# Optimization experiments

Hardware: AMD Instinct MI355X
Metric: run time of the kernel (lower is better)

The kernel has to match this reference:

```python
import jax, jax.numpy as jnp
import numpy as np

C_QKV = 1024
C_HIDDEN = 64
NUM_HEADS = 16
INF = 1e9


def setup_inputs() -> dict:
    key = jax.random.key(0)
    ks = jax.random.split(key, 10)
    B, S = 2, 2048
    d = C_QKV
    hd = C_HIDDEN * NUM_HEADS
    sc = 0.02
    return {
        "input_qkv": jax.random.normal(ks[0], (B, S, d), jnp.float32),
        "mask": jnp.ones((B, 1, 1, S), jnp.float32),
        "bias": jax.random.normal(ks[1], (1, NUM_HEADS, S, S), jnp.float32) * sc,
        "wq": jax.random.normal(ks[2], (d, hd), jnp.float32) * sc,
        "wk": jax.random.normal(ks[3], (d, hd), jnp.float32) * sc,
        "wv": jax.random.normal(ks[4], (d, hd), jnp.float32) * sc,
        "wg": jax.random.normal(ks[5], (d, hd), jnp.float32) * sc,
        "bg": jnp.zeros((hd,), jnp.float32),
        "wo": jax.random.normal(ks[6], (hd, d), jnp.float32) * sc,
        "bo": jnp.zeros((d,), jnp.float32),
    }


def reference(input_qkv, mask, bias, wq, wk, wv, wg, bg, wo, bo):
    B, S, _ = input_qkv.shape
    H, C = NUM_HEADS, C_HIDDEN
    # projections -> [B, H, S, C]
    q = (input_qkv @ wq).reshape(B, S, H, C).transpose(0, 2, 1, 3)
    k = (input_qkv @ wk).reshape(B, S, H, C).transpose(0, 2, 1, 3)
    v = (input_qkv @ wv).reshape(B, S, H, C).transpose(0, 2, 1, 3)
    q = q / jnp.asarray(C, q.dtype) ** 0.5
    # scores [B, H, S, S] with additive mask and pair bias
    a = jnp.einsum("bhqc,bhkc->bhqk", q, k)
    a = a + (mask - 1.0) * INF + bias
    a = jax.nn.softmax(a, axis=-1)
    o = jnp.einsum("bhqk,bhkc->bhqc", a, v).transpose(0, 2, 1, 3)  # [B,S,H,C]
    gate = jax.nn.sigmoid(input_qkv @ wg + bg).reshape(B, S, H, C)
    o = (o * gate).reshape(B, S, H * C)
    return o @ wo + bo
```

## Files before the change

kernel.cpp:

```cpp
#include <hip/hip_runtime.h>
#include <hip/hip_bf16.h>
#include <stdint.h>

typedef unsigned short u16;
typedef __attribute__((ext_vector_type(8))) short short8;
typedef __attribute__((ext_vector_type(4))) short short4v;
typedef __attribute__((ext_vector_type(4))) float f32x4;

#define MFMA16 __builtin_amdgcn_mfma_f32_16x16x32_bf16

#define GLOAD_LDS16(gsrc, ldst) \
  __builtin_amdgcn_global_load_lds((const __attribute__((address_space(1))) void*)(gsrc), \
                                   (__attribute__((address_space(3))) void*)(ldst), 16, 0, 0)

__device__ __forceinline__ u16 f2bf(float x) {
  union { float f; uint32_t u; } v; v.f = x;
  uint32_t r = v.u + 0x7FFFu + ((v.u >> 16) & 1u);
  return (u16)(r >> 16);
}
__device__ __forceinline__ u16 f2bf_rn(float x) {
  __hip_bfloat16 h = __float2bfloat16(x);
  return *reinterpret_cast<u16*>(&h);
}
__device__ __forceinline__ float bf2f(u16 b) {
  union { uint32_t u; float f; } v; v.u = ((uint32_t)b) << 16;
  return v.f;
}

__global__ __launch_bounds__(256) void convert_bf16_kernel(
    const float* __restrict__ in, u16* __restrict__ out, int n) {
  int i = (blockIdx.x * 256 + threadIdx.x) * 8;
  if (i >= n) return;
  float4 a = *(const float4*)(in + i);
  float4 b = *(const float4*)(in + i + 4);
  short8 t;
  t[0] = (short)f2bf(a.x); t[1] = (short)f2bf(a.y);
  t[2] = (short)f2bf(a.z); t[3] = (short)f2bf(a.w);
  t[4] = (short)f2bf(b.x); t[5] = (short)f2bf(b.y);
  t[6] = (short)f2bf(b.z); t[7] = (short)f2bf(b.w);
  *(short8*)(out + i) = t;
}

__global__ __launch_bounds__(256) void transpose_w64_4(
    const float* __restrict__ w0, const float* __restrict__ w1,
    const float* __restrict__ w2, const float* __restrict__ w3,
    u16* __restrict__ WT) {
  __shared__ float tile[64][68];
  const int t = threadIdx.x;
  const int z = blockIdx.z;
  const float* W = (z == 0) ? w0 : (z == 1) ? w1 : (z == 2) ? w2 : w3;
  u16* dst_base = WT + (size_t)z * 1024 * 1024;
  const int k0 = blockIdx.x * 64, n0 = blockIdx.y * 64;
  {
    int r = t >> 2, c0 = (t & 3) * 16;
    const float* src = W + (size_t)(k0 + r) * 1024 + n0 + c0;
#pragma unroll
    for (int j = 0; j < 16; j += 4) {
      float4 v = *(const float4*)(src + j);
      tile[r][c0 + j + 0] = v.x; tile[r][c0 + j + 1] = v.y;
      tile[r][c0 + j + 2] = v.z; tile[r][c0 + j + 3] = v.w;
    }
  }
  __syncthreads();
  {
    int n = t >> 2, kq = (t & 3) * 16;
    short8 t0, t1;
#pragma unroll
    for (int j = 0; j < 8; ++j)  t0[j] = (short)f2bf(tile[kq + j][n]);
#pragma unroll
    for (int j = 0; j < 8; ++j)  t1[j] = (short)f2bf(tile[kq + 8 + j][n]);
    u16* dst = dst_base + (size_t)(n0 + n) * 1024 + k0 + kq;
    *(short8*)dst = t0;
    *(short8*)(dst + 8) = t1;
  }
}

__global__ __launch_bounds__(256) void transpose_w64(
    const float* __restrict__ W, u16* __restrict__ WT, int KK, int NN) {
  __shared__ float tile[64][68];
  const int t = threadIdx.x;
  const int k0 = blockIdx.x * 64, n0 = blockIdx.y * 64;
  {
    int r = t >> 2, c0 = (t & 3) * 16;
    const float* src = W + (size_t)(k0 + r) * NN + n0 + c0;
#pragma unroll
    for (int j = 0; j < 16; j += 4) {
      float4 v = *(const float4*)(src + j);
      tile[r][c0 + j + 0] = v.x; tile[r][c0 + j + 1] = v.y;
      tile[r][c0 + j + 2] = v.z; tile[r][c0 + j + 3] = v.w;
    }
  }
  __syncthreads();
  {
    int n = t >> 2, kq = (t & 3) * 16;
    short8 t0, t1;
#pragma unroll
    for (int j = 0; j < 8; ++j)  t0[j] = (short)f2bf(tile[kq + j][n]);
#pragma unroll
    for (int j = 0; j < 8; ++j)  t1[j] = (short)f2bf(tile[kq + 8 + j][n]);
    u16* dst = WT + (size_t)(n0 + n) * KK + k0 + kq;
    *(short8*)dst = t0;
    *(short8*)(dst + 8) = t1;
  }
}

__global__ __launch_bounds__(256) void transpose_v64(
    const u16* __restrict__ vin, u16* __restrict__ vout) {
  __shared__ u16 tile[64][80];
  const int t = threadIdx.x;
  const int s0 = blockIdx.x * 64;
  const int bh = blockIdx.y;
  const int b = bh >> 4, h = bh & 15;
  {
    int r = t >> 2, c0 = (t & 3) * 16;
    const u16* src = vin + (size_t)(b * 2048 + s0 + r) * 1024 + h * 64 + c0;
    *(short8*)&tile[r][c0] = *(const short8*)src;
    *(short8*)&tile[r][c0 + 8] = *(const short8*)(src + 8);
  }
  __syncthreads();
  {
    int c = t >> 2, s4 = (t & 3) * 16;
    short8 t0, t1;
#pragma unroll
    for (int j = 0; j < 8; ++j) t0[j] = (short)tile[s4 + j][c];
#pragma unroll
    for (int j = 0; j < 8; ++j) t1[j] = (short)tile[s4 + 8 + j][c];
    u16* dst = vout + (size_t)(bh * 64 + c) * 2048 + s0 + s4;
    *(short8*)dst = t0;
    *(short8*)(dst + 8) = t1;
  }
}

__global__ __launch_bounds__(256) void gemm_bt128(
    const u16* __restrict__ A, const u16* __restrict__ BTbase,
    void* __restrict__ dstbase, const float* __restrict__ bvec, int mode) {
  const int K = 1024;
  const int tid = threadIdx.x, lane = tid & 63, w = tid >> 6;
  const int wr = w >> 1, wc = w & 1;
  const int l15 = lane & 15, lg = lane >> 4;
  const int z = (mode < 0) ? (int)blockIdx.z : mode;
  const u16* BT = (mode < 0) ? BTbase + (size_t)z * 1024 * 1024 : BTbase;
  const int rbase = blockIdx.x * 128;
  const int nbase = blockIdx.y * 128;
  __shared__ u16 lsA[128 * 64];
  __shared__ u16 lsB[128 * 64];
  f32x4 acc[4][4] = {};
  const int col8 = (lane & 7) * 8;
  for (int kt = 0; kt < K / 64; ++kt) {
#pragma unroll
    for (int i = 0; i < 4; ++i) {
      int row = w * 32 + i * 8 + (lane >> 3);
      const u16* sa = A + (size_t)(rbase + row) * K + kt * 64 + col8;
      GLOAD_LDS16(sa, lsA + (w * 32 + i * 8) * 64 + lane * 8);
      const u16* sb = BT + (size_t)(nbase + row) * K + kt * 64 + col8;
      GLOAD_LDS16(sb, lsB + (w * 32 + i * 8) * 64 + lane * 8);
    }
    __syncthreads();
#pragma unroll
    for (int kk = 0; kk < 2; ++kk) {
      short8 af[4], bfr[4];
#pragma unroll
      for (int m = 0; m < 4; ++m)
        af[m] = *(const short8*)&lsA[(wr * 64 + m * 16 + l15) * 64 + kk * 32 + lg * 8];
#pragma unroll
      for (int n = 0; n < 4; ++n)
        bfr[n] = *(const short8*)&lsB[(wc * 64 + n * 16 + l15) * 64 + kk * 32 + lg * 8];
#pragma unroll
      for (int m = 0; m < 4; ++m)
#pragma unroll
        for (int n = 0; n < 4; ++n)
          acc[m][n] = MFMA16(af[m], bfr[n], acc[m][n], 0, 0, 0);
    }
    __syncthreads();
  }
  const int r0 = rbase + wr * 64;
  const int c0 = nbase + wc * 64;
  if (z == 4) {
    float* out = (float*)dstbase;
#pragma unroll
    for (int m = 0; m < 4; ++m)
#pragma unroll
      for (int n = 0; n < 4; ++n)
#pragma unroll
        for (int i = 0; i < 4; ++i) {
          int r = r0 + m * 16 + lg * 4 + i;
          int c = c0 + n * 16 + l15;
          out[(size_t)r * 1024 + c] = acc[m][n][i] + bvec[c];
        }
  } else {
    u16* dq = (u16*)dstbase + (size_t)z * 4096 * 1024;
#pragma unroll
    for (int m = 0; m < 4; ++m)
#pragma unroll
      for (int n = 0; n < 4; ++n)
#pragma unroll
        for (int i = 0; i < 4; ++i) {
          int r = r0 + m * 16 + lg * 4 + i;
          int c = c0 + n * 16 + l15;
          float v = acc[m][n][i];
          if (z == 0) v *= 0.125f;
          else if (z == 3) v = 1.f / (1.f + __expf(-(v + bvec[c])));
          dq[(size_t)r * 1024 + c] = f2bf(v);
        }
  }
}

__global__ __launch_bounds__(256, 2) void attn_kernel(
    const u16* __restrict__ qws, const u16* __restrict__ kws,
    const u16* __restrict__ vt, const u16* __restrict__ gws,
    const float* __restrict__ bias, const float* __restrict__ mask,
    u16* __restrict__ og) {
  const int tid = threadIdx.x;
  const int lane = tid & 63;
  const int w = tid >> 6;
  const int l15 = lane & 15, lg = lane >> 4;
  const int bx = blockIdx.x;
  const int qt = (bx & 7) | ((bx >> 4) << 3);
  const int b = (bx >> 3) & 1;
  const int h = blockIdx.y;

  __shared__ __align__(16) u16 ring[3][8192];
  __shared__ __align__(16) u16 lsP[4][2304];
  __shared__ __align__(16) u16 lsM[2048];

  const float* bias_base = bias + ((size_t)h * 2048 + qt * 128) * 2048;
  const u16* vt_base = vt + (size_t)((b * 16 + h) * 64) * 2048;
  const u16* k_base = kws + (size_t)(b * 2048) * 1024 + h * 64;

  {
    float4 m0 = *(const float4*)(mask + b * 2048 + tid * 8);
    float4 m1 = *(const float4*)(mask + b * 2048 + tid * 8 + 4);
    short8 mm;
    mm[0] = (short)f2bf((m0.x - 1.f) * 1e9f); mm[1] = (short)f2bf((m0.y - 1.f) * 1e9f);
    mm[2] = (short)f2bf((m0.z - 1.f) * 1e9f); mm[3] = (short)f2bf((m0.w - 1.f) * 1e9f);
    mm[4] = (short)f2bf((m1.x - 1.f) * 1e9f); mm[5] = (short)f2bf((m1.y - 1.f) * 1e9f);
    mm[6] = (short)f2bf((m1.z - 1.f) * 1e9f); mm[7] = (short)f2bf((m1.w - 1.f) * 1e9f);
    *(short8*)&lsM[tid * 8] = mm;
  }

  const size_t qrow0 = (size_t)(b * 2048 + qt * 128 + w * 32 + l15) * 1024 + h * 64;
  const size_t qrow1 = qrow0 + 16 * 1024;
  short8 qf00 = *(const short8*)(qws + qrow0 + lg * 8);
  short8 qf01 = *(const short8*)(qws + qrow0 + 32 + lg * 8);
  short8 qf10 = *(const short8*)(qws + qrow1 + lg * 8);
  short8 qf11 = *(const short8*)(qws + qrow1 + 32 + lg * 8);
  asm volatile("" :: "v"(qf00), "v"(qf01), "v"(qf10), "v"(qf11));
  asm volatile("s_waitcnt vmcnt(0)" ::: "memory");
  __builtin_amdgcn_sched_barrier(0);

  f32x4 O[2][4] = {};
  float lacc0 = 0.f, lacc1 = 0.f;
  f32x4 bA0, bA1, bA2, bA3, bA4, bA5, bA6, bA7;
  f32x4 bB0, bB1, bB2, bB3, bB4, bB5, bB6, bB7;
  f32x4 kX0, kX1, vX0, vX1, kY0, kY1, vY0, vY1;

#define STAGE_ISSUE(K0, K1, V0, V1, KW) {                                           \
    int r_ = tid >> 3, cg_ = tid & 7;                                               \
    const u16* kp_ = k_base + (size_t)((KW) * 64 + r_) * 1024 + cg_ * 8;            \
    const u16* vp_ = vt_base + (size_t)r_ * 2048 + (KW) * 64 + cg_ * 8;             \
    asm volatile("global_load_dwordx4 %0, %1, off" : "=v"(K0) : "v"(kp_));          \
    asm volatile("global_load_dwordx4 %0, %1, off" : "=v"(K1) : "v"(kp_ + 32 * 1024)); \
    asm volatile("global_load_dwordx4 %0, %1, off" : "=v"(V0) : "v"(vp_));          \
    asm volatile("global_load_dwordx4 %0, %1, off" : "=v"(V1) : "v"(vp_ + 32 * 2048)); \
  }

#define STAGE_WRITE(SLOT, K0, K1, V0, V1) {                                         \
    int r_ = tid >> 3, cg_ = tid & 7;                                               \
    int d0_ = (r_ * 8 + (cg_ ^ (r_ & 7))) * 8;                                      \
    int r2_ = r_ + 32;                                                              \
    int d1_ = (r2_ * 8 + (cg_ ^ (r2_ & 7))) * 8;                                    \
    *(f32x4*)&ring[SLOT][d0_] = K0;                                                 \
    *(f32x4*)&ring[SLOT][d1_] = K1;                                                 \
    *(f32x4*)&ring[SLOT][4096 + d0_] = V0;                                          \
    *(f32x4*)&ring[SLOT][4096 + d1_] = V1;                                          \
  }

#define BIAS_ISSUE(R0, R1, R2, R3, R4, R5, R6, R7, KW) {                            \
    const float* bp_ = bias_base + (size_t)(w * 32 + l15) * 2048 + (KW) * 64 + lg * 4; \
    asm volatile("global_load_dwordx4 %0, %1, off" : "=v"(R0) : "v"(bp_));          \
    asm volatile("global_load_dwordx4 %0, %1, off" : "=v"(R1) : "v"(bp_ + 16));     \
    asm volatile("global_load_dwordx4 %0, %1, off" : "=v"(R2) : "v"(bp_ + 32));     \
    asm volatile("global_load_dwordx4 %0, %1, off" : "=v"(R3) : "v"(bp_ + 48));     \
    asm volatile("global_load_dwordx4 %0, %1, off" : "=v"(R4) : "v"(bp_ + 16 * 2048)); \
    asm volatile("global_load_dwordx4 %0, %1, off" : "=v"(R5) : "v"(bp_ + 16 * 2048 + 16)); \
    asm volatile("global_load_dwordx4 %0, %1, off" : "=v"(R6) : "v"(bp_ + 16 * 2048 + 32)); \
    asm volatile("global_load_dwordx4 %0, %1, off" : "=v"(R7) : "v"(bp_ + 16 * 2048 + 48)); \
  }

#define COMPUTE(SLOT, KB, X0, X1, X2, X3, X4, X5, X6, X7) {                         \
    const u16* Kc_ = &ring[SLOT][0];                                                \
    const u16* Vc_ = &ring[SLOT][4096];                                             \
    f32x4 bb0[4] = {X0, X1, X2, X3};                                                \
    f32x4 bb1[4] = {X4, X5, X6, X7};                                                \
    f32x4 s_[2][4];                                                                 \
    _Pragma("unroll") for (int kt = 0; kt < 4; ++kt) {                              \
      int krow_ = kt * 16 + l15;                                                    \
      int sw_ = krow_ & 7;                                                          \
      short8 kfa_ = *(const short8*)&Kc_[(krow_ * 8 + (lg ^ sw_)) * 8];             \
      short8 kfb_ = *(const short8*)&Kc_[(krow_ * 8 + ((4 + lg) ^ sw_)) * 8];       \
      short4v mk_ = *(const short4v*)&lsM[(KB) * 64 + kt * 16 + lg * 4];            \
      f32x4 ci0_, ci1_;                                                             \
      _Pragma("unroll") for (int i = 0; i < 4; ++i) {                               \
        float m_ = bf2f((u16)mk_[i]);                                               \
        ci0_[i] = bb0[kt][i] + m_;                                                  \
        ci1_[i] = bb1[kt][i] + m_;                                                  \
      }                                                                             \
      s_[0][kt] = MFMA16(kfa_, qf00, ci0_, 0, 0, 0);                                \
      s_[0][kt] = MFMA16(kfb_, qf01, s_[0][kt], 0, 0, 0);                           \
      s_[1][kt] = MFMA16(kfa_, qf10, ci1_, 0, 0, 0);                                \
      s_[1][kt] = MFMA16(kfb_, qf11, s_[1][kt], 0, 0, 0);                           \
    }                                                                               \
    _Pragma("unroll") for (int kt = 0; kt < 4; ++kt) {                              \
      short4v p0_, p1_;                                                             \
      _Pragma("unroll") for (int i = 0; i < 4; ++i) {                               \
        float e0_ = __expf(s_[0][kt][i]); lacc0 += e0_; p0_[i] = (short)f2bf_rn(e0_); \
        float e1_ = __expf(s_[1][kt][i]); lacc1 += e1_; p1_[i] = (short)f2bf_rn(e1_); \
      }                                                                             \
      *(short4v*)&lsP[w][(l15) * 72 + kt * 16 + lg * 4] = p0_;                      \
      *(short4v*)&lsP[w][(16 + l15) * 72 + kt * 16 + lg * 4] = p1_;                 \
    }                                                                               \
    short8 pf00_ = *(const short8*)&lsP[w][(l15) * 72 + lg * 8];                    \
    short8 pf01_ = *(const short8*)&lsP[w][(l15) * 72 + 32 + lg * 8];               \
    short8 pf10_ = *(const short8*)&lsP[w][(16 + l15) * 72 + lg * 8];               \
    short8 pf11_ = *(const short8*)&lsP[w][(16 + l15) * 72 + 32 + lg * 8];          \
    _Pragma("unroll") for (int cf = 0; cf < 4; ++cf) {                              \
      int c_ = cf * 16 + l15;                                                       \
      int sw_ = c_ & 7;                                                             \
      short8 vf0_ = *(const short8*)&Vc_[(c_ * 8 + (lg ^ sw_)) * 8];                \
      short8 vf1_ = *(const short8*)&Vc_[(c_ * 8 + ((4 + lg) ^ sw_)) * 8];          \
      O[0][cf] = MFMA16(vf0_, pf00_, O[0][cf], 0, 0, 0);                            \
      O[0][cf] = MFMA16(vf1_, pf01_, O[0][cf], 0, 0, 0);                            \
      O[1][cf] = MFMA16(vf0_, pf10_, O[1][cf], 0, 0, 0);                            \
      O[1][cf] = MFMA16(vf1_, pf11_, O[1][cf], 0, 0, 0);                            \
    } }

#define BODY(KB, N, SK0, SK1, SV0, SV1, TK0, TK1, TV0, TV1,                         \
             X0, X1, X2, X3, X4, X5, X6, X7) {                                      \
    if ((KB) + 2 < 32) STAGE_ISSUE(SK0, SK1, SV0, SV1, (KB) + 2);                   \
    COMPUTE((KB) % 3, KB, X0, X1, X2, X3, X4, X5, X6, X7);                          \
    if ((KB) + 2 < 32) BIAS_ISSUE(X0, X1, X2, X3, X4, X5, X6, X7, (KB) + 2);        \
    asm volatile("s_waitcnt vmcnt(" #N ")" ::: "memory");                           \
    __builtin_amdgcn_sched_barrier(0);                                              \
    if ((KB) + 1 < 32) {                                                            \
      STAGE_WRITE(((KB) + 1) % 3, TK0, TK1, TV0, TV1);                              \
      asm volatile("s_waitcnt lgkmcnt(0)" ::: "memory");                            \
      __builtin_amdgcn_sched_barrier(0);                                            \
      __builtin_amdgcn_s_barrier();                                                 \
    } }

  STAGE_ISSUE(kX0, kX1, vX0, vX1, 0);
  BIAS_ISSUE(bA0, bA1, bA2, bA3, bA4, bA5, bA6, bA7, 0);
  STAGE_ISSUE(kY0, kY1, vY0, vY1, 1);
  BIAS_ISSUE(bB0, bB1, bB2, bB3, bB4, bB5, bB6, bB7, 1);
  asm volatile("s_waitcnt vmcnt(12)" ::: "memory");
  __builtin_amdgcn_sched_barrier(0);
  STAGE_WRITE(0, kX0, kX1, vX0, vX1);
  asm volatile("s_waitcnt lgkmcnt(0)" ::: "memory");
  __builtin_amdgcn_sched_barrier(0);
  __builtin_amdgcn_s_barrier();

  for (int kb2 = 0; kb2 < 30; kb2 += 2) {
    BODY(kb2,     12, kX0, kX1, vX0, vX1, kY0, kY1, vY0, vY1,
         bA0, bA1, bA2, bA3, bA4, bA5, bA6, bA7);
    BODY(kb2 + 1, 12, kY0, kY1, vY0, vY1, kX0, kX1, vX0, vX1,
         bB0, bB1, bB2, bB3, bB4, bB5, bB6, bB7);
  }
  BODY(30, 0, kX0, kX1, vX0, vX1, kY0, kY1, vY0, vY1,
       bA0, bA1, bA2, bA3, bA4, bA5, bA6, bA7);
  BODY(31, 0, kY0, kY1, vY0, vY1, kX0, kX1, vX0, vX1,
       bB0, bB1, bB2, bB3, bB4, bB5, bB6, bB7);

  lacc0 += __shfl_xor(lacc0, 16); lacc0 += __shfl_xor(lacc0, 32);
  lacc1 += __shfl_xor(lacc1, 16); lacc1 += __shfl_xor(lacc1, 32);
  {
    float inv0 = 1.f / lacc0, inv1 = 1.f / lacc1;
#pragma unroll
    for (int cf = 0; cf < 4; ++cf) {
      short4v ga = *(const short4v*)(gws + qrow0 + cf * 16 + lg * 4);
      short4v gb = *(const short4v*)(gws + qrow1 + cf * 16 + lg * 4);
      short4v oa, ob;
#pragma unroll
      for (int i = 0; i < 4; ++i) {
        oa[i] = (short)f2bf_rn(O[0][cf][i] * inv0 * bf2f((u16)ga[i]));
        ob[i] = (short)f2bf_rn(O[1][cf][i] * inv1 * bf2f((u16)gb[i]));
      }
      *(short4v*)(og + qrow0 + cf * 16 + lg * 4) = oa;
      *(short4v*)(og + qrow1 + cf * 16 + lg * 4) = ob;
    }
  }
#undef STAGE_ISSUE
#undef STAGE_WRITE
#undef BIAS_ISSUE
#undef COMPUTE
#undef BODY
}

extern "C" void kernel_launch(void* const* d_in, const int* in_sizes, int n_in,
                              void* d_out, int out_size, void* d_ws, size_t ws_size,
                              hipStream_t stream) {
  const float* x    = (const float*)d_in[0];
  const float* mask = (const float*)d_in[1];
  const float* bias = (const float*)d_in[2];
  const float* wq   = (const float*)d_in[3];
  const float* wk   = (const float*)d_in[4];
  const float* wv   = (const float*)d_in[5];
  const float* wg   = (const float*)d_in[6];
  const float* bg   = (const float*)d_in[7];
  const float* wo   = (const float*)d_in[8];
  const float* bo   = (const float*)d_in[9];
  float* out = (float*)d_out;

  char* ws = (char*)d_ws;
  const size_t MB = 1ull << 20;
  u16* xb   = (u16*)(ws + 0);
  u16* wt   = (u16*)(ws + 8 * MB);
  u16* wot  = (u16*)(ws + 16 * MB);
  u16* proj = (u16*)(ws + 18 * MB);
  u16* vtp  = (u16*)(ws + 50 * MB);
  u16* og   = (u16*)(ws + 58 * MB);
  const size_t PSZ = (size_t)4096 * 1024;

  convert_bf16_kernel<<<2048, 256, 0, stream>>>(x, xb, 4096 * 1024);

  transpose_w64_4<<<dim3(16, 16, 4), 256, 0, stream>>>(wq, wk, wv, wg, wt);
  transpose_w64<<<dim3(16, 16), 256, 0, stream>>>(wo, wot, 1024, 1024);

  gemm_bt128<<<dim3(32, 8, 4), 256, 0, stream>>>(xb, wt, (void*)proj, bg, -1);

  transpose_v64<<<dim3(32, 32), 256, 0, stream>>>(proj + 2 * PSZ, vtp);

  attn_kernel<<<dim3(32, 16), 256, 0, stream>>>(proj, proj + PSZ, vtp, proj + 3 * PSZ,
                                                bias, mask, og);

  gemm_bt128<<<dim3(32, 8, 1), 256, 0, stream>>>(og, wot, (void*)out, bo, 4);
}
```

Measured before the change: 207.5 us.

## Process both batches per attention block to share bias tiles on-CU

The attention kernel now launches 512-thread blocks in which the two groups of four waves handle batch 0 and batch 1 for the same head and query tile. Since the pair bias does not depend on batch, both groups read identical bias addresses, which should hit in the same CU's cache instead of relying on L2 locality between separate blocks. The K/V ring, P scratch and mask buffers are doubled to hold both batches, which raises LDS use to roughly 142KB per block and limits residency to one block per CU. The wider launch bound may also tighten the per-thread register budget.

```diff
diff --git a/kernel.cpp b/kernel.cpp
--- a/kernel.cpp
+++ b/kernel.cpp
@@ -205,7 +205,7 @@
   }
 }
 
-__global__ __launch_bounds__(256, 2) void attn_kernel(
+__global__ __launch_bounds__(512, 2) void attn_kernel(
     const u16* __restrict__ qws, const u16* __restrict__ kws,
     const u16* __restrict__ vt, const u16* __restrict__ gws,
     const float* __restrict__ bias, const float* __restrict__ mask,
@@ -213,23 +213,25 @@
   const int tid = threadIdx.x;
   const int lane = tid & 63;
   const int w = tid >> 6;
+  const int bb = w >> 2;
+  const int ws = w & 3;
   const int l15 = lane & 15, lg = lane >> 4;
-  const int bx = blockIdx.x;
-  const int qt = (bx & 7) | ((bx >> 4) << 3);
-  const int b = (bx >> 3) & 1;
+  const int qt = blockIdx.x;
   const int h = blockIdx.y;
 
-  __shared__ __align__(16) u16 ring[3][8192];
-  __shared__ __align__(16) u16 lsP[4][2304];
-  __shared__ __align__(16) u16 lsM[2048];
+  __shared__ __align__(16) u16 ring[3][16384];
+  __shared__ __align__(16) u16 lsP[8][2304];
+  __shared__ __align__(16) u16 lsM[4096];
 
   const float* bias_base = bias + ((size_t)h * 2048 + qt * 128) * 2048;
-  const u16* vt_base = vt + (size_t)((b * 16 + h) * 64) * 2048;
-  const u16* k_base = kws + (size_t)(b * 2048) * 1024 + h * 64;
-
-  {
-    float4 m0 = *(const float4*)(mask + b * 2048 + tid * 8);
-    float4 m1 = *(const float4*)(mask + b * 2048 + tid * 8 + 4);
+  const u16* k_base0 = kws + (size_t)h * 64;
+  const u16* k_base1 = kws + (size_t)2048 * 1024 + h * 64;
+  const u16* vt_base0 = vt + (size_t)(h * 64) * 2048;
+  const u16* vt_base1 = vt + (size_t)((16 + h) * 64) * 2048;
+
+  {
+    float4 m0 = *(const float4*)(mask + tid * 8);
+    float4 m1 = *(const float4*)(mask + tid * 8 + 4);
     short8 mm;
     mm[0] = (short)f2bf((m0.x - 1.f) * 1e9f); mm[1] = (short)f2bf((m0.y - 1.f) * 1e9f);
     mm[2] = (short)f2bf((m0.z - 1.f) * 1e9f); mm[3] = (short)f2bf((m0.w - 1.f) * 1e9f);
@@ -238,7 +240,7 @@
     *(short8*)&lsM[tid * 8] = mm;
   }
 
-  const size_t qrow0 = (size_t)(b * 2048 + qt * 128 + w * 32 + l15) * 1024 + h * 64;
+  const size_t qrow0 = (size_t)(bb * 2048 + qt * 128 + ws * 32 + l15) * 1024 + h * 64;
   const size_t qrow1 = qrow0 + 16 * 1024;
   short8 qf00 = *(const short8*)(qws + qrow0 + lg * 8);
   short8 qf01 = *(const short8*)(qws + qrow0 + 32 + lg * 8);
@@ -256,27 +258,27 @@
 
 #define STAGE_ISSUE(K0, K1, V0, V1, KW) {                                           \
     int r_ = tid >> 3, cg_ = tid & 7;                                               \
-    const u16* kp_ = k_base + (size_t)((KW) * 64 + r_) * 1024 + cg_ * 8;            \
-    const u16* vp_ = vt_base + (size_t)r_ * 2048 + (KW) * 64 + cg_ * 8;             \
-    asm volatile("global_load_dwordx4 %0, %1, off" : "=v"(K0) : "v"(kp_));          \
-    asm volatile("global_load_dwordx4 %0, %1, off" : "=v"(K1) : "v"(kp_ + 32 * 1024)); \
-    asm volatile("global_load_dwordx4 %0, %1, off" : "=v"(V0) : "v"(vp_));          \
-    asm volatile("global_load_dwordx4 %0, %1, off" : "=v"(V1) : "v"(vp_ + 32 * 2048)); \
+    const u16* kp0 = k_base0 + (size_t)((KW) * 64 + r_) * 1024 + cg_ * 8;           \
+    const u16* kp1 = k_base1 + (size_t)((KW) * 64 + r_) * 1024 + cg_ * 8;           \
+    const u16* vp0 = vt_base0 + (size_t)r_ * 2048 + (KW) * 64 + cg_ * 8;            \
+    const u16* vp1 = vt_base1 + (size_t)r_ * 2048 + (KW) * 64 + cg_ * 8;            \
+    asm volatile("global_load_dwordx4 %0, %1, off" : "=v"(K0) : "v"(kp0));          \
+    asm volatile("global_load_dwordx4 %0, %1, off" : "=v"(K1) : "v"(kp1));          \
+    asm volatile("global_load_dwordx4 %0, %1, off" : "=v"(V0) : "v"(vp0));          \
+    asm volatile("global_load_dwordx4 %0, %1, off" : "=v"(V1) : "v"(vp1));          \
   }
 
 #define STAGE_WRITE(SLOT, K0, K1, V0, V1) {                                         \
     int r_ = tid >> 3, cg_ = tid & 7;                                               \
     int d0_ = (r_ * 8 + (cg_ ^ (r_ & 7))) * 8;                                      \
-    int r2_ = r_ + 32;                                                              \
-    int d1_ = (r2_ * 8 + (cg_ ^ (r2_ & 7))) * 8;                                    \
     *(f32x4*)&ring[SLOT][d0_] = K0;                                                 \
-    *(f32x4*)&ring[SLOT][d1_] = K1;                                                 \
     *(f32x4*)&ring[SLOT][4096 + d0_] = V0;                                          \
-    *(f32x4*)&ring[SLOT][4096 + d1_] = V1;                                          \
+    *(f32x4*)&ring[SLOT][8192 + d0_] = K1;                                          \
+    *(f32x4*)&ring[SLOT][12288 + d0_] = V1;                                         \
   }
 
 #define BIAS_ISSUE(R0, R1, R2, R3, R4, R5, R6, R7, KW) {                            \
-    const float* bp_ = bias_base + (size_t)(w * 32 + l15) * 2048 + (KW) * 64 + lg * 4; \
+    const float* bp_ = bias_base + (size_t)(ws * 32 + l15) * 2048 + (KW) * 64 + lg * 4; \
     asm volatile("global_load_dwordx4 %0, %1, off" : "=v"(R0) : "v"(bp_));          \
     asm volatile("global_load_dwordx4 %0, %1, off" : "=v"(R1) : "v"(bp_ + 16));     \
     asm volatile("global_load_dwordx4 %0, %1, off" : "=v"(R2) : "v"(bp_ + 32));     \
@@ -288,8 +290,8 @@
   }
 
 #define COMPUTE(SLOT, KB, X0, X1, X2, X3, X4, X5, X6, X7) {                         \
-    const u16* Kc_ = &ring[SLOT][0];                                                \
-    const u16* Vc_ = &ring[SLOT][4096];                                             \
+    const u16* Kc_ = &ring[SLOT][bb * 8192];                                        \
+    const u16* Vc_ = &ring[SLOT][bb * 8192 + 4096];                                 \
     f32x4 bb0[4] = {X0, X1, X2, X3};                                                \
     f32x4 bb1[4] = {X4, X5, X6, X7};                                                \
     f32x4 s_[2][4];                                                                 \
@@ -298,7 +300,7 @@
       int sw_ = krow_ & 7;                                                          \
       short8 kfa_ = *(const short8*)&Kc_[(krow_ * 8 + (lg ^ sw_)) * 8];             \
       short8 kfb_ = *(const short8*)&Kc_[(krow_ * 8 + ((4 + lg) ^ sw_)) * 8];       \
-      short4v mk_ = *(const short4v*)&lsM[(KB) * 64 + kt * 16 + lg * 4];            \
+      short4v mk_ = *(const short4v*)&lsM[bb * 2048 + (KB) * 64 + kt * 16 + lg * 4]; \
       f32x4 ci0_, ci1_;                                                             \
       _Pragma("unroll") for (int i = 0; i < 4; ++i) {                               \
         float m_ = bf2f((u16)mk_[i]);                                               \
@@ -334,15 +336,15 @@
       O[1][cf] = MFMA16(vf1_, pf11_, O[1][cf], 0, 0, 0);                            \
     } }
 
-#define BODY(KB, N, SK0, SK1, SV0, SV1, TK0, TK1, TV0, TV1,                         \
+#define BODY(KB, N, ISK0, ISK1, ISV0, ISV1, WRK0, WRK1, WRV0, WRV1,                 \
              X0, X1, X2, X3, X4, X5, X6, X7) {                                      \
-    if ((KB) + 2 < 32) STAGE_ISSUE(SK0, SK1, SV0, SV1, (KB) + 2);                   \
+    if ((KB) + 2 < 32) STAGE_ISSUE(ISK0, ISK1, ISV0, ISV1, (KB) + 2);               \
     COMPUTE((KB) % 3, KB, X0, X1, X2, X3, X4, X5, X6, X7);                          \
     if ((KB) + 2 < 32) BIAS_ISSUE(X0, X1, X2, X3, X4, X5, X6, X7, (KB) + 2);        \
     asm volatile("s_waitcnt vmcnt(" #N ")" ::: "memory");                           \
     __builtin_amdgcn_sched_barrier(0);                                              \
     if ((KB) + 1 < 32) {                                                            \
-      STAGE_WRITE(((KB) + 1) % 3, TK0, TK1, TV0, TV1);                              \
+      STAGE_WRITE(((KB) + 1) % 3, WRK0, WRK1, WRV0, WRV1);                          \
       asm volatile("s_waitcnt lgkmcnt(0)" ::: "memory");                            \
       __builtin_amdgcn_sched_barrier(0);                                            \
       __builtin_amdgcn_s_barrier();                                                 \
@@ -429,7 +431,7 @@
 
   transpose_v64<<<dim3(32, 32), 256, 0, stream>>>(proj + 2 * PSZ, vtp);
 
-  attn_kernel<<<dim3(32, 16), 256, 0, stream>>>(proj, proj + PSZ, vtp, proj + 3 * PSZ,
+  attn_kernel<<<dim3(16, 16), 512, 0, stream>>>(proj, proj + PSZ, vtp, proj + 3 * PSZ,
                                                 bias, mask, og);
 
   gemm_bt128<<<dim3(32, 8, 1), 256, 0, stream>>>(og, wot, (void*)out, bo, 4);
```

After: 210.1 us. About the same (+1.3%).

## Split attention key range across two blocks and combine partials in a new kernel

Applied to the files above, without the earlier changes.

The attention kernel now processes only half of the 2048 keys per block, with a batch/split index on grid z. This doubles the block count. Each block also starts its key walk at a per-head/per-tile rotated window. The block writes unnormalized fp32 partial outputs and row sums to workspace, and a new combine kernel adds the two halves, normalizes, applies the gate and writes bf16. The aim is more parallelism and spread-out memory access, at the cost of extra fp32 partial traffic and a launch. It also drops the earlier block ordering that kept both batches' reads of the same bias tile close in time.

```diff
diff --git a/kernel.cpp b/kernel.cpp
--- a/kernel.cpp
+++ b/kernel.cpp
@@ -207,29 +207,33 @@
 
 __global__ __launch_bounds__(256, 2) void attn_kernel(
     const u16* __restrict__ qws, const u16* __restrict__ kws,
-    const u16* __restrict__ vt, const u16* __restrict__ gws,
-    const float* __restrict__ bias, const float* __restrict__ mask,
-    u16* __restrict__ og) {
+    const u16* __restrict__ vt, const float* __restrict__ bias,
+    const float* __restrict__ mask, float* __restrict__ opart,
+    float* __restrict__ lpart) {
   const int tid = threadIdx.x;
   const int lane = tid & 63;
   const int w = tid >> 6;
   const int l15 = lane & 15, lg = lane >> 4;
-  const int bx = blockIdx.x;
-  const int qt = (bx & 7) | ((bx >> 4) << 3);
-  const int b = (bx >> 3) & 1;
+  const int qt = blockIdx.x;
   const int h = blockIdx.y;
+  const int bz = blockIdx.z;
+  const int bb = bz >> 1;
+  const int ks = bz & 1;
+  const int kb0 = ((h << 1) | (qt >> 3)) & 15;
+
+#define KWIN(KB) (ks * 16 + (((KB) + kb0) & 15))
 
   __shared__ __align__(16) u16 ring[3][8192];
   __shared__ __align__(16) u16 lsP[4][2304];
   __shared__ __align__(16) u16 lsM[2048];
 
   const float* bias_base = bias + ((size_t)h * 2048 + qt * 128) * 2048;
-  const u16* vt_base = vt + (size_t)((b * 16 + h) * 64) * 2048;
-  const u16* k_base = kws + (size_t)(b * 2048) * 1024 + h * 64;
-
-  {
-    float4 m0 = *(const float4*)(mask + b * 2048 + tid * 8);
-    float4 m1 = *(const float4*)(mask + b * 2048 + tid * 8 + 4);
+  const u16* vt_base = vt + (size_t)((bb * 16 + h) * 64) * 2048;
+  const u16* k_base = kws + (size_t)(bb * 2048) * 1024 + h * 64;
+
+  {
+    float4 m0 = *(const float4*)(mask + bb * 2048 + tid * 8);
+    float4 m1 = *(const float4*)(mask + bb * 2048 + tid * 8 + 4);
     short8 mm;
     mm[0] = (short)f2bf((m0.x - 1.f) * 1e9f); mm[1] = (short)f2bf((m0.y - 1.f) * 1e9f);
     mm[2] = (short)f2bf((m0.z - 1.f) * 1e9f); mm[3] = (short)f2bf((m0.w - 1.f) * 1e9f);
@@ -238,7 +242,7 @@
     *(short8*)&lsM[tid * 8] = mm;
   }
 
-  const size_t qrow0 = (size_t)(b * 2048 + qt * 128 + w * 32 + l15) * 1024 + h * 64;
+  const size_t qrow0 = (size_t)(bb * 2048 + qt * 128 + w * 32 + l15) * 1024 + h * 64;
   const size_t qrow1 = qrow0 + 16 * 1024;
   short8 qf00 = *(const short8*)(qws + qrow0 + lg * 8);
   short8 qf01 = *(const short8*)(qws + qrow0 + 32 + lg * 8);
@@ -254,10 +258,11 @@
   f32x4 bB0, bB1, bB2, bB3, bB4, bB5, bB6, bB7;
   f32x4 kX0, kX1, vX0, vX1, kY0, kY1, vY0, vY1;
 
-#define STAGE_ISSUE(K0, K1, V0, V1, KW) {                                           \
+#define STAGE_ISSUE(K0, K1, V0, V1, KB) {                                           \
+    int kw_ = KWIN(KB);                                                             \
     int r_ = tid >> 3, cg_ = tid & 7;                                               \
-    const u16* kp_ = k_base + (size_t)((KW) * 64 + r_) * 1024 + cg_ * 8;            \
-    const u16* vp_ = vt_base + (size_t)r_ * 2048 + (KW) * 64 + cg_ * 8;             \
+    const u16* kp_ = k_base + (size_t)(kw_ * 64 + r_) * 1024 + cg_ * 8;             \
+    const u16* vp_ = vt_base + (size_t)r_ * 2048 + kw_ * 64 + cg_ * 8;              \
     asm volatile("global_load_dwordx4 %0, %1, off" : "=v"(K0) : "v"(kp_));          \
     asm volatile("global_load_dwordx4 %0, %1, off" : "=v"(K1) : "v"(kp_ + 32 * 1024)); \
     asm volatile("global_load_dwordx4 %0, %1, off" : "=v"(V0) : "v"(vp_));          \
@@ -275,8 +280,8 @@
     *(f32x4*)&ring[SLOT][4096 + d1_] = V1;                                          \
   }
 
-#define BIAS_ISSUE(R0, R1, R2, R3, R4, R5, R6, R7, KW) {                            \
-    const float* bp_ = bias_base + (size_t)(w * 32 + l15) * 2048 + (KW) * 64 + lg * 4; \
+#define BIAS_ISSUE(R0, R1, R2, R3, R4, R5, R6, R7, KB) {                            \
+    const float* bp_ = bias_base + (size_t)(w * 32 + l15) * 2048 + KWIN(KB) * 64 + lg * 4; \
     asm volatile("global_load_dwordx4 %0, %1, off" : "=v"(R0) : "v"(bp_));          \
     asm volatile("global_load_dwordx4 %0, %1, off" : "=v"(R1) : "v"(bp_ + 16));     \
     asm volatile("global_load_dwordx4 %0, %1, off" : "=v"(R2) : "v"(bp_ + 32));     \
@@ -290,20 +295,20 @@
 #define COMPUTE(SLOT, KB, X0, X1, X2, X3, X4, X5, X6, X7) {                         \
     const u16* Kc_ = &ring[SLOT][0];                                                \
     const u16* Vc_ = &ring[SLOT][4096];                                             \
-    f32x4 bb0[4] = {X0, X1, X2, X3};                                                \
-    f32x4 bb1[4] = {X4, X5, X6, X7};                                                \
+    f32x4 bb0_[4] = {X0, X1, X2, X3};                                               \
+    f32x4 bb1_[4] = {X4, X5, X6, X7};                                               \
     f32x4 s_[2][4];                                                                 \
     _Pragma("unroll") for (int kt = 0; kt < 4; ++kt) {                              \
       int krow_ = kt * 16 + l15;                                                    \
       int sw_ = krow_ & 7;                                                          \
       short8 kfa_ = *(const short8*)&Kc_[(krow_ * 8 + (lg ^ sw_)) * 8];             \
       short8 kfb_ = *(const short8*)&Kc_[(krow_ * 8 + ((4 + lg) ^ sw_)) * 8];       \
-      short4v mk_ = *(const short4v*)&lsM[(KB) * 64 + kt * 16 + lg * 4];            \
+      short4v mk_ = *(const short4v*)&lsM[KWIN(KB) * 64 + kt * 16 + lg * 4];        \
       f32x4 ci0_, ci1_;                                                             \
       _Pragma("unroll") for (int i = 0; i < 4; ++i) {                               \
         float m_ = bf2f((u16)mk_[i]);                                               \
-        ci0_[i] = bb0[kt][i] + m_;                                                  \
-        ci1_[i] = bb1[kt][i] + m_;                                                  \
+        ci0_[i] = bb0_[kt][i] + m_;                                                 \
+        ci1_[i] = bb1_[kt][i] + m_;                                                 \
       }                                                                             \
       s_[0][kt] = MFMA16(kfa_, qf00, ci0_, 0, 0, 0);                                \
       s_[0][kt] = MFMA16(kfb_, qf01, s_[0][kt], 0, 0, 0);                           \
@@ -334,15 +339,15 @@
       O[1][cf] = MFMA16(vf1_, pf11_, O[1][cf], 0, 0, 0);                            \
     } }
 
-#define BODY(KB, N, SK0, SK1, SV0, SV1, TK0, TK1, TV0, TV1,                         \
+#define BODY(KB, N, ISK0, ISK1, ISV0, ISV1, WRK0, WRK1, WRV0, WRV1,                 \
              X0, X1, X2, X3, X4, X5, X6, X7) {                                      \
-    if ((KB) + 2 < 32) STAGE_ISSUE(SK0, SK1, SV0, SV1, (KB) + 2);                   \
+    if ((KB) + 2 < 16) STAGE_ISSUE(ISK0, ISK1, ISV0, ISV1, (KB) + 2);               \
     COMPUTE((KB) % 3, KB, X0, X1, X2, X3, X4, X5, X6, X7);                          \
-    if ((KB) + 2 < 32) BIAS_ISSUE(X0, X1, X2, X3, X4, X5, X6, X7, (KB) + 2);        \
+    if ((KB) + 2 < 16) BIAS_ISSUE(X0, X1, X2, X3, X4, X5, X6, X7, (KB) + 2);        \
     asm volatile("s_waitcnt vmcnt(" #N ")" ::: "memory");                           \
     __builtin_amdgcn_sched_barrier(0);                                              \
-    if ((KB) + 1 < 32) {                                                            \
-      STAGE_WRITE(((KB) + 1) % 3, TK0, TK1, TV0, TV1);                              \
+    if ((KB) + 1 < 16) {                                                            \
+      STAGE_WRITE(((KB) + 1) % 3, WRK0, WRK1, WRV0, WRV1);                          \
       asm volatile("s_waitcnt lgkmcnt(0)" ::: "memory");                            \
       __builtin_amdgcn_sched_barrier(0);                                            \
       __builtin_amdgcn_s_barrier();                                                 \
@@ -359,40 +364,75 @@
   __builtin_amdgcn_sched_barrier(0);
   __builtin_amdgcn_s_barrier();
 
-  for (int kb2 = 0; kb2 < 30; kb2 += 2) {
+  for (int kb2 = 0; kb2 < 14; kb2 += 2) {
     BODY(kb2,     12, kX0, kX1, vX0, vX1, kY0, kY1, vY0, vY1,
          bA0, bA1, bA2, bA3, bA4, bA5, bA6, bA7);
     BODY(kb2 + 1, 12, kY0, kY1, vY0, vY1, kX0, kX1, vX0, vX1,
          bB0, bB1, bB2, bB3, bB4, bB5, bB6, bB7);
   }
-  BODY(30, 0, kX0, kX1, vX0, vX1, kY0, kY1, vY0, vY1,
+  BODY(14, 0, kX0, kX1, vX0, vX1, kY0, kY1, vY0, vY1,
        bA0, bA1, bA2, bA3, bA4, bA5, bA6, bA7);
-  BODY(31, 0, kY0, kY1, vY0, vY1, kX0, kX1, vX0, vX1,
+  BODY(15, 0, kY0, kY1, vY0, vY1, kX0, kX1, vX0, vX1,
        bB0, bB1, bB2, bB3, bB4, bB5, bB6, bB7);
 
   lacc0 += __shfl_xor(lacc0, 16); lacc0 += __shfl_xor(lacc0, 32);
   lacc1 += __shfl_xor(lacc1, 16); lacc1 += __shfl_xor(lacc1, 32);
-  {
-    float inv0 = 1.f / lacc0, inv1 = 1.f / lacc1;
-#pragma unroll
-    for (int cf = 0; cf < 4; ++cf) {
-      short4v ga = *(const short4v*)(gws + qrow0 + cf * 16 + lg * 4);
-      short4v gb = *(const short4v*)(gws + qrow1 + cf * 16 + lg * 4);
-      short4v oa, ob;
-#pragma unroll
-      for (int i = 0; i < 4; ++i) {
-        oa[i] = (short)f2bf_rn(O[0][cf][i] * inv0 * bf2f((u16)ga[i]));
-        ob[i] = (short)f2bf_rn(O[1][cf][i] * inv1 * bf2f((u16)gb[i]));
-      }
-      *(short4v*)(og + qrow0 + cf * 16 + lg * 4) = oa;
-      *(short4v*)(og + qrow1 + cf * 16 + lg * 4) = ob;
-    }
+  if (lg == 0) {
+    float* lp = lpart + (size_t)ks * 65536 +
+                (size_t)(bb * 2048 + qt * 128 + w * 32 + l15) * 16 + h;
+    lp[0] = lacc0;
+    lp[16 * 16] = lacc1;
+  }
+  __syncthreads();
+  float* ob = (float*)&ring[0][0];
+#pragma unroll
+  for (int qa = 0; qa < 2; ++qa)
+#pragma unroll
+    for (int cf = 0; cf < 4; ++cf)
+#pragma unroll
+      for (int i = 0; i < 4; ++i)
+        ob[(w * 32 + qa * 16 + l15) * 68 + cf * 16 + lg * 4 + i] = O[qa][cf][i];
+  __syncthreads();
+  {
+    int q2 = tid >> 1, c0 = (tid & 1) * 32;
+    float* dst = opart + (size_t)ks * 4194304 +
+                 (size_t)(bb * 2048 + qt * 128 + q2) * 1024 + h * 64 + c0;
+#pragma unroll
+    for (int j = 0; j < 8; ++j)
+      *(f32x4*)(dst + j * 4) = *(const f32x4*)&ob[q2 * 68 + c0 + j * 4];
   }
 #undef STAGE_ISSUE
 #undef STAGE_WRITE
 #undef BIAS_ISSUE
 #undef COMPUTE
 #undef BODY
+#undef KWIN
+}
+
+__global__ __launch_bounds__(256) void combine_kernel(
+    const float* __restrict__ opart, const float* __restrict__ lpart,
+    const u16* __restrict__ gws, u16* __restrict__ og) {
+  int t = blockIdx.x * 256 + threadIdx.x;
+  int row = t >> 7;
+  int rem = (t * 8) & 1023;
+  int h = rem >> 6;
+  const float* p0 = opart + (size_t)row * 1024 + rem;
+  const float* p1 = p0 + 4194304;
+  float4 a0 = *(const float4*)p0, a1 = *(const float4*)(p0 + 4);
+  float4 b0 = *(const float4*)p1, b1 = *(const float4*)(p1 + 4);
+  float l = lpart[row * 16 + h] + lpart[65536 + row * 16 + h];
+  float inv = 1.f / l;
+  short8 g8 = *(const short8*)(gws + (size_t)row * 1024 + rem);
+  short8 o8;
+  o8[0] = (short)f2bf_rn((a0.x + b0.x) * inv * bf2f((u16)g8[0]));
+  o8[1] = (short)f2bf_rn((a0.y + b0.y) * inv * bf2f((u16)g8[1]));
+  o8[2] = (short)f2bf_rn((a0.z + b0.z) * inv * bf2f((u16)g8[2]));
+  o8[3] = (short)f2bf_rn((a0.w + b0.w) * inv * bf2f((u16)g8[3]));
+  o8[4] = (short)f2bf_rn((a1.x + b1.x) * inv * bf2f((u16)g8[4]));
+  o8[5] = (short)f2bf_rn((a1.y + b1.y) * inv * bf2f((u16)g8[5]));
+  o8[6] = (short)f2bf_rn((a1.z + b1.z) * inv * bf2f((u16)g8[6]));
+  o8[7] = (short)f2bf_rn((a1.w + b1.w) * inv * bf2f((u16)g8[7]));
+  *(short8*)(og + (size_t)row * 1024 + rem) = o8;
 }
 
 extern "C" void kernel_launch(void* const* d_in, const int* in_sizes, int n_in,
@@ -412,12 +452,14 @@
 
   char* ws = (char*)d_ws;
   const size_t MB = 1ull << 20;
-  u16* xb   = (u16*)(ws + 0);
-  u16* wt   = (u16*)(ws + 8 * MB);
-  u16* wot  = (u16*)(ws + 16 * MB);
-  u16* proj = (u16*)(ws + 18 * MB);
-  u16* vtp  = (u16*)(ws + 50 * MB);
-  u16* og   = (u16*)(ws + 58 * MB);
+  u16* xb    = (u16*)(ws + 0);
+  u16* wt    = (u16*)(ws + 8 * MB);
+  u16* wot   = (u16*)(ws + 16 * MB);
+  u16* proj  = (u16*)(ws + 18 * MB);
+  u16* vtp   = (u16*)(ws + 50 * MB);
+  u16* og    = (u16*)(ws + 58 * MB);
+  float* opart = (float*)(ws + 66 * MB);
+  float* lpart = (float*)(ws + 98 * MB);
   const size_t PSZ = (size_t)4096 * 1024;
 
   convert_bf16_kernel<<<2048, 256, 0, stream>>>(x, xb, 4096 * 1024);
@@ -429,8 +471,10 @@
 
   transpose_v64<<<dim3(32, 32), 256, 0, stream>>>(proj + 2 * PSZ, vtp);
 
-  attn_kernel<<<dim3(32, 16), 256, 0, stream>>>(proj, proj + PSZ, vtp, proj + 3 * PSZ,
-                                                bias, mask, og);
+  attn_kernel<<<dim3(16, 16, 4), 256, 0, stream>>>(proj, proj + PSZ, vtp,
+                                                   bias, mask, opart, lpart);
+
+  combine_kernel<<<2048, 256, 0, stream>>>(opart, lpart, proj + 3 * PSZ, og);
 
   gemm_bt128<<<dim3(32, 8, 1), 256, 0, stream>>>(og, wot, (void*)out, bo, 4);
 }
```

Result: slower. 250.6 us (+20.7%).
